# Kernel tuning notes

Hardware: AMD Instinct MI355X
Metric: run time of the kernel (lower is better)

The kernel has to match this reference:

```python
import jax, jax.numpy as jnp
import numpy as np

B, S, E, H = 2, 2048, 1024, 16
HD = E // H  # 64
NEG = -1e24


def setup_inputs() -> dict:
    key = jax.random.key(0)
    ks = jax.random.split(key, 20)
    sc_e = 1.0 / np.sqrt(E)
    inp = {
        "q_matrix": jax.random.normal(ks[0], (B, S, E), jnp.float32),
        "k_matrix": jax.random.normal(ks[1], (B, S, E), jnp.float32),
        "v_matrix": jax.random.normal(ks[2], (B, S, E), jnp.float32),
        "mask": jax.random.randint(ks[3], (B, S, S), 0, 2).astype(bool),
        # global QKV projections (embed_dim -> embed_dim)
        "Wq": jax.random.normal(ks[4], (E, E), jnp.float32) * sc_e,
        "bq": jnp.zeros((E,), jnp.float32),
        "Wk": jax.random.normal(ks[5], (E, E), jnp.float32) * sc_e,
        "bk": jnp.zeros((E,), jnp.float32),
        "Wv": jax.random.normal(ks[6], (E, E), jnp.float32) * sc_e,
        "bv": jnp.zeros((E,), jnp.float32),
        # per-head QKV projections (embed_dim -> head_dim), batched over heads
        "Whq": jax.random.normal(ks[7], (H, E, HD), jnp.float32) * sc_e,
        "bhq": jnp.zeros((H, HD), jnp.float32),
        "Whk": jax.random.normal(ks[8], (H, E, HD), jnp.float32) * sc_e,
        "bhk": jnp.zeros((H, HD), jnp.float32),
        "Whv": jax.random.normal(ks[9], (H, E, HD), jnp.float32) * sc_e,
        "bhv": jnp.zeros((H, HD), jnp.float32),
        # output projection
        "Wo": jax.random.normal(ks[10], (E, E), jnp.float32) * sc_e,
        "bo": jnp.zeros((E,), jnp.float32),
    }
    return inp


def reference(q_matrix, k_matrix, v_matrix, mask, Wq, bq, Wk, bk, Wv, bv,
              Whq, bhq, Whk, bhk, Whv, bhv, Wo, bo):
    # global projections [B,S,E]
    qg = q_matrix @ Wq + bq
    kg = k_matrix @ Wk + bk
    vg = v_matrix @ Wv + bv
    # per-head projections -> [B,H,S,HD]
    qh = jnp.einsum('bse,hed->bhsd', qg, Whq) + bhq[None, :, None, :]
    kh = jnp.einsum('bse,hed->bhsd', kg, Whk) + bhk[None, :, None, :]
    vh = jnp.einsum('bse,hed->bhsd', vg, Whv) + bhv[None, :, None, :]
    # scaled dot-product attention, scores [B,H,S,S]
    scores = jnp.einsum('bhsd,bhtd->bhst', qh, kh) / jnp.sqrt(jnp.float32(HD))
    scores = jnp.where(mask[:, None, :, :], NEG, scores)
    weights = jax.nn.softmax(scores, axis=-1)
    out = jnp.einsum('bhst,bhtd->bhsd', weights, vh)
    # concat heads (head order along last dim, matching torch.cat)
    x = out.transpose(0, 2, 1, 3).reshape(out.shape[0], out.shape[2], E)
    return x @ Wo + bo
```

## Files before the change

### kernel.cpp

```cpp
#include <hip/hip_runtime.h>
#include <hip/hip_bf16.h>

typedef unsigned short us16;
typedef __attribute__((ext_vector_type(8))) short short8;
typedef __attribute__((ext_vector_type(4))) float float4v;

#define E_DIM 1024
#define S_LEN 2048
#define B_DIM 2
#define H_DIM 16
#define HD_DIM 64
#define M_ROWS 4096

__device__ __forceinline__ us16 f2b(float f) {
    unsigned int u = __float_as_uint(f);
    unsigned int r = (u + 0x7fffu + ((u >> 16) & 1u)) >> 16;
    return (us16)r;
}
__device__ __forceinline__ us16 f2b_fast(float f) {
    return (us16)((__float_as_uint(f) + 0x8000u) >> 16);
}

__device__ __forceinline__ void gload16(const us16* g, us16* lds_uniform_base) {
    __builtin_amdgcn_global_load_lds(
        (const __attribute__((address_space(1))) void*)g,
        (__attribute__((address_space(3))) void*)lds_uniform_base, 16, 0, 0);
}

__global__ void zero_f32(float* p, int n) {
    int i = blockIdx.x * 256 + threadIdx.x;
    if (i < n) p[i] = 0.f;
}

__global__ void convert6(const float* s0, const float* s1, const float* s2,
                         const float* s3, const float* s4, const float* s5,
                         us16* d0, us16* d1, us16* d2,
                         us16* d3, us16* d4, us16* d5) {
    int z = blockIdx.y;
    const float* in = z == 0 ? s0 : z == 1 ? s1 : z == 2 ? s2 : z == 3 ? s3 : z == 4 ? s4 : s5;
    us16* out = z == 0 ? d0 : z == 1 ? d1 : z == 2 ? d2 : z == 3 ? d3 : z == 4 ? d4 : d5;
    int n = (z < 3) ? (M_ROWS * E_DIM) : (E_DIM * E_DIM);
    int idx = (blockIdx.x * 256 + threadIdx.x) * 8;
    if (idx >= n) return;
    float4 f0 = *(const float4*)(in + idx);
    float4 f1 = *(const float4*)(in + idx + 4);
    us16 t[8] = {f2b(f0.x), f2b(f0.y), f2b(f0.z), f2b(f0.w),
                 f2b(f1.x), f2b(f1.y), f2b(f1.z), f2b(f1.w)};
    *(uint4*)(out + idx) = *(const uint4*)t;
}

__global__ void transpose4(const float* __restrict__ s0, const float* __restrict__ s1,
                           const float* __restrict__ s2, const float* __restrict__ s3,
                           us16* __restrict__ d0, us16* __restrict__ d1,
                           us16* __restrict__ d2, us16* __restrict__ d3) {
    __shared__ us16 tile[32][33];
    int z = blockIdx.z;
    const float* in = z == 0 ? s0 : z == 1 ? s1 : z == 2 ? s2 : s3;
    us16* out = z == 0 ? d0 : z == 1 ? d1 : z == 2 ? d2 : d3;
    int mode = (z < 3) ? 1 : 0;
    int bx = blockIdx.x, by = blockIdx.y;
    int tx = threadIdx.x, ty = threadIdx.y;
#pragma unroll
    for (int i = 0; i < 4; ++i) {
        int e = by * 32 + ty + i * 8;
        int c = bx * 32 + tx;
        size_t src;
        if (mode == 0) src = (size_t)e * E_DIM + c;
        else           src = ((size_t)(c >> 6) * E_DIM + e) * 64 + (c & 63);
        tile[ty + i * 8][tx] = f2b(in[src]);
    }
    __syncthreads();
#pragma unroll
    for (int i = 0; i < 4; ++i) {
        int c = bx * 32 + ty + i * 8;
        int e = by * 32 + tx;
        out[(size_t)c * E_DIM + e] = tile[tx][ty + i * 8];
    }
}

__global__ void bias_combine3(const float* g0, const float* g1, const float* g2,
                              const float* W0, const float* W1, const float* W2,
                              const float* h0, const float* h1, const float* h2,
                              float* c0, float* c1, float* c2) {
    int z = blockIdx.y;
    const float* bg = z == 0 ? g0 : z == 1 ? g1 : g2;
    const float* Wh = z == 0 ? W0 : z == 1 ? W1 : W2;
    const float* bh = z == 0 ? h0 : z == 1 ? h1 : h2;
    float* bc = z == 0 ? c0 : z == 1 ? c1 : c2;
    int h = blockIdx.x;
    int tid = threadIdx.x;
    int d = tid & 63, part = tid >> 6;
    float acc = 0.f;
    int j0 = part * 256;
    for (int j = j0; j < j0 + 256; ++j)
        acc += bg[j] * Wh[((size_t)h * E_DIM + j) * HD_DIM + d];
    __shared__ float red[4][64];
    red[part][d] = acc;
    __syncthreads();
    if (tid < 64)
        bc[h * 64 + tid] = red[0][tid] + red[1][tid] + red[2][tid] + red[3][tid] + bh[h * 64 + tid];
}

__global__ void mask_pack(const int* __restrict__ mask, unsigned long long* __restrict__ bits) {
    int row = blockIdx.x * 4 + (threadIdx.x >> 6);
    int lane = threadIdx.x & 63;
    const int* mp = mask + (size_t)row * S_LEN;
    for (int w = 0; w < 32; ++w) {
        int mv = mp[w * 64 + lane];
        unsigned long long bal = __ballot(mv != 0);
        if (lane == 0) bits[(size_t)row * 32 + w] = bal;
    }
}

#define BK 32

__device__ __forceinline__ void gemm_body(
    const us16* __restrict__ A, const us16* __restrict__ Bt,
    const float* __restrict__ bias, void* __restrict__ Cp,
    int M, int N, int K, int bxt, int byt, int omode)
{
    __shared__ us16 As[128 * BK];
    __shared__ us16 Bs[128 * BK];

    int tid = threadIdx.x;
    int wave = tid >> 6, lane = tid & 63;
    int quad = lane >> 4, l16 = lane & 15;
    int wm = (wave >> 1) * 64, wn = (wave & 1) * 64;
    int bm0 = byt * 128, bn0 = bxt * 128;
    int srow = lane >> 2;
    int gcol = (((lane & 3) ^ (srow & 3)) << 3);
    int rslot = ((quad ^ (l16 & 3)) << 3);

    float4v acc[4][4];
#pragma unroll
    for (int i = 0; i < 4; ++i)
#pragma unroll
        for (int j = 0; j < 4; ++j)
#pragma unroll
            for (int r = 0; r < 4; ++r) acc[i][j][r] = 0.f;

    for (int k0 = 0; k0 < K; k0 += BK) {
#pragma unroll
        for (int c = 0; c < 2; ++c) {
            int r0 = 32 * wave + 16 * c;
            gload16(A  + (size_t)(bm0 + r0 + srow) * K + k0 + gcol, &As[r0 * BK]);
            gload16(Bt + (size_t)(bn0 + r0 + srow) * K + k0 + gcol, &Bs[r0 * BK]);
        }
        __syncthreads();
        short8 af[4], bfr[4];
#pragma unroll
        for (int i = 0; i < 4; ++i)
            af[i] = *(const short8*)&As[(wm + i * 16 + l16) * BK + rslot];
#pragma unroll
        for (int j = 0; j < 4; ++j)
            bfr[j] = *(const short8*)&Bs[(wn + j * 16 + l16) * BK + rslot];
#pragma unroll
        for (int i = 0; i < 4; ++i)
#pragma unroll
            for (int j = 0; j < 4; ++j)
                acc[i][j] = __builtin_amdgcn_mfma_f32_16x16x32_bf16(af[i], bfr[j], acc[i][j], 0, 0, 0);
        __syncthreads();
    }

#pragma unroll
    for (int i = 0; i < 4; ++i) {
#pragma unroll
        for (int j = 0; j < 4; ++j) {
#pragma unroll
            for (int r = 0; r < 4; ++r) {
                int row = bm0 + wm + i * 16 + quad * 4 + r;
                int col = bn0 + wn + j * 16 + l16;
                float v = acc[i][j][r] + ((omode == 3) ? bias[row] : bias[col]);
                if (omode == 0) {
                    ((us16*)Cp)[(size_t)row * N + col] = f2b(v);
                } else if (omode == 1) {
                    int b = row >> 11, s = row & 2047, h = col >> 6, d = col & 63;
                    ((us16*)Cp)[(((size_t)(b * H_DIM + h) * S_LEN + s) * HD_DIM) + d] = f2b(v);
                } else if (omode == 2) {
                    ((float*)Cp)[(size_t)row * N + col] = v;
                } else {
                    int h = row >> 6, d = row & 63, b = col >> 11, sl = col & 2047;
                    ((us16*)Cp)[(((size_t)(b * H_DIM + h) * HD_DIM + d) * S_LEN) + sl] = f2b(v);
                }
            }
        }
    }
}

__global__ __launch_bounds__(256) void wgemm3(
    const us16* A0, const us16* A1, const us16* A2,
    const us16* B0, const us16* B1, const us16* B2,
    const float* zbias, us16* C0, us16* C1, us16* C2)
{
    int z = blockIdx.z;
    const us16* A = z == 0 ? A0 : z == 1 ? A1 : A2;
    const us16* Bt = z == 0 ? B0 : z == 1 ? B1 : B2;
    us16* C = z == 0 ? C0 : z == 1 ? C1 : C2;
    gemm_body(A, Bt, zbias, C, E_DIM, E_DIM, E_DIM, blockIdx.x, blockIdx.y, 0);
}

__global__ __launch_bounds__(256) void proj_all(
    const us16* __restrict__ qb, const us16* __restrict__ kb, const us16* __restrict__ vb,
    const us16* __restrict__ WcqT, const us16* __restrict__ WckT, const us16* __restrict__ WcvT,
    const float* __restrict__ bcq, const float* __restrict__ bck, const float* __restrict__ bcv,
    us16* __restrict__ qhb, us16* __restrict__ khb, us16* __restrict__ vtb)
{
    int bx = blockIdx.x;
    int z = bx >> 8, t = bx & 255;
    if (z == 0)      gemm_body(qb, WcqT, bcq, qhb, M_ROWS, E_DIM, E_DIM, t & 7, t >> 3, 1);
    else if (z == 1) gemm_body(kb, WckT, bck, khb, M_ROWS, E_DIM, E_DIM, t & 7, t >> 3, 1);
    else             gemm_body(WcvT, vb, bcv, vtb, E_DIM, M_ROWS, E_DIM, t & 31, t >> 5, 3);
}

__global__ __launch_bounds__(256) void gemm_out64(
    const us16* __restrict__ A, const us16* __restrict__ Bt,
    const float* __restrict__ bias, float* __restrict__ C,
    int M, int N, int K)
{
    __shared__ us16 As[64 * BK];
    __shared__ us16 Bs[128 * BK];

    int tid = threadIdx.x;
    int wave = tid >> 6, lane = tid & 63;
    int quad = lane >> 4, l16 = lane & 15;
    int wm = (wave >> 1) * 32, wn = (wave & 1) * 64;
    int bm0 = blockIdx.y * 64, bn0 = blockIdx.x * 128;
    int srow = lane >> 2;
    int gcol = (((lane & 3) ^ (srow & 3)) << 3);
    int rslot = ((quad ^ (l16 & 3)) << 3);

    float4v acc[2][4];
#pragma unroll
    for (int i = 0; i < 2; ++i)
#pragma unroll
        for (int j = 0; j < 4; ++j)
#pragma unroll
            for (int r = 0; r < 4; ++r) acc[i][j][r] = 0.f;

    for (int k0 = 0; k0 < K; k0 += BK) {
        gload16(A + (size_t)(bm0 + 16 * wave + srow) * K + k0 + gcol, &As[16 * wave * BK]);
#pragma unroll
        for (int c = 0; c < 2; ++c) {
            int r0 = 32 * wave + 16 * c;
            gload16(Bt + (size_t)(bn0 + r0 + srow) * K + k0 + gcol, &Bs[r0 * BK]);
        }
        __syncthreads();
        short8 af[2], bfr[4];
#pragma unroll
        for (int i = 0; i < 2; ++i)
            af[i] = *(const short8*)&As[(wm + i * 16 + l16) * BK + rslot];
#pragma unroll
        for (int j = 0; j < 4; ++j)
            bfr[j] = *(const short8*)&Bs[(wn + j * 16 + l16) * BK + rslot];
#pragma unroll
        for (int i = 0; i < 2; ++i)
#pragma unroll
            for (int j = 0; j < 4; ++j)
                acc[i][j] = __builtin_amdgcn_mfma_f32_16x16x32_bf16(af[i], bfr[j], acc[i][j], 0, 0, 0);
        __syncthreads();
    }

#pragma unroll
    for (int i = 0; i < 2; ++i)
#pragma unroll
        for (int j = 0; j < 4; ++j)
#pragma unroll
            for (int r = 0; r < 4; ++r) {
                int row = bm0 + wm + i * 16 + quad * 4 + r;
                int col = bn0 + wn + j * 16 + l16;
                C[(size_t)row * N + col] = acc[i][j][r] + bias[col];
            }
}

#define LDK 72
#define LDP 76
#define SCALE2 0.18033688011112042f

__global__ __launch_bounds__(256) void attn_kernel(
    const us16* __restrict__ qh, const us16* __restrict__ kh,
    const us16* __restrict__ vt, const unsigned long long* __restrict__ mbits,
    us16* __restrict__ x)
{
    __shared__ us16 Ks[64 * LDK];
    __shared__ us16 Vs[64 * LDK];
    __shared__ us16 Pw[4][16 * LDP];

    int tid = threadIdx.x;
    int w = tid >> 6, lane = tid & 63;
    int quad = lane >> 4, l16 = lane & 15;
    int bh = blockIdx.y;
    int b = bh >> 4, h = bh & 15;
    int q0 = blockIdx.x * 64;
    const size_t base = (size_t)bh * (S_LEN * HD_DIM);

    short8 qf0, qf1;
    {
        int qrow = q0 + w * 16 + l16;
        const us16* qp = qh + base + (size_t)qrow * HD_DIM + quad * 8;
        qf0 = *(const short8*)qp;
        qf1 = *(const short8*)(qp + 32);
    }

    float l_i[4];
    float4v o[4];
#pragma unroll
    for (int r = 0; r < 4; ++r) l_i[r] = 0.f;
#pragma unroll
    for (int dt = 0; dt < 4; ++dt)
#pragma unroll
        for (int r = 0; r < 4; ++r) o[dt][r] = 0.f;

    int qb = q0 + w * 16 + quad * 4;
    const unsigned long long* mrow = mbits + (size_t)(b * S_LEN + qb) * 32;

    for (int kt = 0; kt < S_LEN; kt += 64) {
        __syncthreads();
#pragma unroll
        for (int it = 0; it < 2; ++it) {
            int c = tid + it * 256;
            int r = c >> 3, cc = (c & 7) * 8;
            *(uint4*)&Ks[r * LDK + cc] = *(const uint4*)(kh + base + (size_t)(kt + r) * HD_DIM + cc);
            *(uint4*)&Vs[r * LDK + cc] = *(const uint4*)(vt + base + (size_t)r * S_LEN + kt + cc);
        }
        __syncthreads();

        int kw = kt >> 6;
        unsigned long long mw[4];
#pragma unroll
        for (int r = 0; r < 4; ++r) mw[r] = mrow[r * 32 + kw];

        float4v sc[4];
#pragma unroll
        for (int ct = 0; ct < 4; ++ct) {
            short8 kf0 = *(const short8*)&Ks[(ct * 16 + l16) * LDK + quad * 8];
            short8 kf1 = *(const short8*)&Ks[(ct * 16 + l16) * LDK + 32 + quad * 8];
            float4v a;
#pragma unroll
            for (int r = 0; r < 4; ++r) a[r] = 0.f;
            a = __builtin_amdgcn_mfma_f32_16x16x32_bf16(qf0, kf0, a, 0, 0, 0);
            a = __builtin_amdgcn_mfma_f32_16x16x32_bf16(qf1, kf1, a, 0, 0, 0);
            sc[ct] = a;
        }

#pragma unroll
        for (int ct = 0; ct < 4; ++ct) {
            int sh = ct * 16 + l16;
#pragma unroll
            for (int r = 0; r < 4; ++r) {
                float pin = ((mw[r] >> sh) & 1ull) ? -1e38f : sc[ct][r] * SCALE2;
                float p = __builtin_amdgcn_exp2f(pin);
                l_i[r] += p;
                Pw[w][(quad * 4 + r) * LDP + ct * 16 + l16] = f2b_fast(p);
            }
        }

        short8 pf0 = *(const short8*)&Pw[w][l16 * LDP + quad * 8];
        short8 pf1 = *(const short8*)&Pw[w][l16 * LDP + 32 + quad * 8];
#pragma unroll
        for (int dt = 0; dt < 4; ++dt) {
            short8 vf0 = *(const short8*)&Vs[(dt * 16 + l16) * LDK + quad * 8];
            short8 vf1 = *(const short8*)&Vs[(dt * 16 + l16) * LDK + 32 + quad * 8];
            o[dt] = __builtin_amdgcn_mfma_f32_16x16x32_bf16(pf0, vf0, o[dt], 0, 0, 0);
            o[dt] = __builtin_amdgcn_mfma_f32_16x16x32_bf16(pf1, vf1, o[dt], 0, 0, 0);
        }
    }

#pragma unroll
    for (int r = 0; r < 4; ++r) {
        float s = l_i[r];
        s += __shfl_xor(s, 1, 64);
        s += __shfl_xor(s, 2, 64);
        s += __shfl_xor(s, 4, 64);
        s += __shfl_xor(s, 8, 64);
        l_i[r] = 1.0f / s;
    }
#pragma unroll
    for (int dt = 0; dt < 4; ++dt)
#pragma unroll
        for (int r = 0; r < 4; ++r) {
            int s = qb + r;
            int col = h * HD_DIM + dt * 16 + l16;
            x[(size_t)(b * S_LEN + s) * E_DIM + col] = f2b(o[dt][r] * l_i[r]);
        }
}

extern "C" void kernel_launch(void* const* d_in, const int* in_sizes, int n_in,
                              void* d_out, int out_size, void* d_ws, size_t ws_size,
                              hipStream_t stream) {
    const float* q    = (const float*)d_in[0];
    const float* k    = (const float*)d_in[1];
    const float* v    = (const float*)d_in[2];
    const int*   mask = (const int*)d_in[3];
    const float* Wq = (const float*)d_in[4];   const float* bq = (const float*)d_in[5];
    const float* Wk = (const float*)d_in[6];   const float* bk = (const float*)d_in[7];
    const float* Wv = (const float*)d_in[8];   const float* bv = (const float*)d_in[9];
    const float* Whq = (const float*)d_in[10]; const float* bhq = (const float*)d_in[11];
    const float* Whk = (const float*)d_in[12]; const float* bhk = (const float*)d_in[13];
    const float* Whv = (const float*)d_in[14]; const float* bhv = (const float*)d_in[15];
    const float* Wo = (const float*)d_in[16];  const float* bo = (const float*)d_in[17];

    us16* ws = (us16*)d_ws;
    const size_t M1 = (size_t)1 << 20;
    us16* WhqT = ws + 0 * M1;
    us16* WhkT = ws + 1 * M1;
    us16* WhvT = ws + 2 * M1;
    us16* WoT  = ws + 3 * M1;
    us16* WcqT = ws + 4 * M1;
    us16* WckT = ws + 5 * M1;
    us16* WcvT = ws + 6 * M1;
    us16* Wqb  = ws + 7 * M1;
    us16* Wkb  = ws + 8 * M1;
    us16* Wvb  = ws + 9 * M1;
    us16* qb   = ws + 10 * M1;
    us16* kb   = ws + 14 * M1;
    us16* vb   = ws + 18 * M1;
    us16* qhb  = ws + 22 * M1;
    us16* khb  = ws + 26 * M1;
    us16* vtb  = ws + 30 * M1;
    us16* xb   = vb;
    float* bcq   = (float*)(ws + 34 * M1);
    float* bck   = bcq + 1024;
    float* bcv   = bck + 1024;
    float* zbias = bcv + 1024;
    unsigned long long* mbits = (unsigned long long*)(ws + 34 * M1 + 16384);

    zero_f32<<<4, 256, 0, stream>>>(zbias, 1024);
    bias_combine3<<<dim3(H_DIM, 3), 256, 0, stream>>>(bq, bk, bv, Whq, Whk, Whv,
                                                      bhq, bhk, bhv, bcq, bck, bcv);
    transpose4<<<dim3(32, 32, 4), dim3(32, 8), 0, stream>>>(Whq, Whk, Whv, Wo,
                                                            WhqT, WhkT, WhvT, WoT);
    mask_pack<<<1024, 256, 0, stream>>>(mask, mbits);
    convert6<<<dim3(2048, 6), 256, 0, stream>>>(q, k, v, Wq, Wk, Wv,
                                                qb, kb, vb, Wqb, Wkb, Wvb);

    wgemm3<<<dim3(8, 8, 3), 256, 0, stream>>>(WhqT, WhkT, WhvT, Wqb, Wkb, Wvb, zbias,
                                              WcqT, WckT, WcvT);

    proj_all<<<768, 256, 0, stream>>>(qb, kb, vb, WcqT, WckT, WcvT,
                                      bcq, bck, bcv, qhb, khb, vtb);

    attn_kernel<<<dim3(32, 32), 256, 0, stream>>>(qhb, khb, vtb, mbits, xb);

    gemm_out64<<<dim3(8, 64), 256, 0, stream>>>(xb, WoT, bo, (float*)d_out,
                                                M_ROWS, E_DIM, E_DIM);
}
```

Baseline: 372.7 us.

## Merge prep kernels, split attention over key halves, use 64-row weight GEMM

Five small preprocessing launches (bf16 conversion, weight transposes, mask packing, bias combine, zeroing) become a single `prep` kernel dispatched by block index. The weight-combining GEMM moves to a 64-row tile body to launch more blocks. Attention splits the key range into two halves along a new grid dimension, with 512-thread blocks covering 128 queries. It writes unnormalized partial outputs and row sums, and a new `attn_combine` kernel adds the halves and normalizes. This aims to raise occupancy and parallelism and cut launch overhead, at the cost of extra partial-result memory traffic and one more launch. The combine step only adds partial sums, so it is only correct if the attention does not rely on a per-half running max.

```diff
diff --git a/kernel.cpp b/kernel.cpp
--- a/kernel.cpp
+++ b/kernel.cpp
@@ -12,6 +12,9 @@
 #define HD_DIM 64
 #define M_ROWS 4096
 
+__device__ __forceinline__ float b2f(us16 b) {
+    return __uint_as_float(((unsigned int)b) << 16);
+}
 __device__ __forceinline__ us16 f2b(float f) {
     unsigned int u = __float_as_uint(f);
     unsigned int r = (u + 0x7fffu + ((u >> 16) & 1u)) >> 16;
@@ -27,88 +30,91 @@
         (__attribute__((address_space(3))) void*)lds_uniform_base, 16, 0, 0);
 }
 
-__global__ void zero_f32(float* p, int n) {
-    int i = blockIdx.x * 256 + threadIdx.x;
-    if (i < n) p[i] = 0.f;
-}
-
-__global__ void convert6(const float* s0, const float* s1, const float* s2,
-                         const float* s3, const float* s4, const float* s5,
-                         us16* d0, us16* d1, us16* d2,
-                         us16* d3, us16* d4, us16* d5) {
-    int z = blockIdx.y;
-    const float* in = z == 0 ? s0 : z == 1 ? s1 : z == 2 ? s2 : z == 3 ? s3 : z == 4 ? s4 : s5;
-    us16* out = z == 0 ? d0 : z == 1 ? d1 : z == 2 ? d2 : z == 3 ? d3 : z == 4 ? d4 : d5;
-    int n = (z < 3) ? (M_ROWS * E_DIM) : (E_DIM * E_DIM);
-    int idx = (blockIdx.x * 256 + threadIdx.x) * 8;
-    if (idx >= n) return;
-    float4 f0 = *(const float4*)(in + idx);
-    float4 f1 = *(const float4*)(in + idx + 4);
-    us16 t[8] = {f2b(f0.x), f2b(f0.y), f2b(f0.z), f2b(f0.w),
-                 f2b(f1.x), f2b(f1.y), f2b(f1.z), f2b(f1.w)};
-    *(uint4*)(out + idx) = *(const uint4*)t;
-}
-
-__global__ void transpose4(const float* __restrict__ s0, const float* __restrict__ s1,
-                           const float* __restrict__ s2, const float* __restrict__ s3,
-                           us16* __restrict__ d0, us16* __restrict__ d1,
-                           us16* __restrict__ d2, us16* __restrict__ d3) {
+__global__ __launch_bounds__(256) void prep(
+    const float* __restrict__ q, const float* __restrict__ k, const float* __restrict__ v,
+    const float* __restrict__ Wq, const float* __restrict__ Wk, const float* __restrict__ Wv,
+    const float* __restrict__ Whq, const float* __restrict__ Whk, const float* __restrict__ Whv,
+    const float* __restrict__ Wo,
+    const float* __restrict__ bq, const float* __restrict__ bk, const float* __restrict__ bv,
+    const float* __restrict__ bhq, const float* __restrict__ bhk, const float* __restrict__ bhv,
+    const int* __restrict__ mask,
+    us16* qb, us16* kb, us16* vb, us16* Wqb, us16* Wkb, us16* Wvb,
+    us16* WhqT, us16* WhkT, us16* WhvT, us16* WoT,
+    unsigned long long* mbits,
+    float* bcq, float* bck, float* bcv, float* zbias)
+{
     __shared__ us16 tile[32][33];
-    int z = blockIdx.z;
-    const float* in = z == 0 ? s0 : z == 1 ? s1 : z == 2 ? s2 : s3;
-    us16* out = z == 0 ? d0 : z == 1 ? d1 : z == 2 ? d2 : d3;
-    int mode = (z < 3) ? 1 : 0;
-    int bx = blockIdx.x, by = blockIdx.y;
-    int tx = threadIdx.x, ty = threadIdx.y;
-#pragma unroll
-    for (int i = 0; i < 4; ++i) {
-        int e = by * 32 + ty + i * 8;
-        int c = bx * 32 + tx;
-        size_t src;
-        if (mode == 0) src = (size_t)e * E_DIM + c;
-        else           src = ((size_t)(c >> 6) * E_DIM + e) * 64 + (c & 63);
-        tile[ty + i * 8][tx] = f2b(in[src]);
-    }
-    __syncthreads();
-#pragma unroll
-    for (int i = 0; i < 4; ++i) {
-        int c = bx * 32 + ty + i * 8;
-        int e = by * 32 + tx;
-        out[(size_t)c * E_DIM + e] = tile[tx][ty + i * 8];
-    }
-}
-
-__global__ void bias_combine3(const float* g0, const float* g1, const float* g2,
-                              const float* W0, const float* W1, const float* W2,
-                              const float* h0, const float* h1, const float* h2,
-                              float* c0, float* c1, float* c2) {
-    int z = blockIdx.y;
-    const float* bg = z == 0 ? g0 : z == 1 ? g1 : g2;
-    const float* Wh = z == 0 ? W0 : z == 1 ? W1 : W2;
-    const float* bh = z == 0 ? h0 : z == 1 ? h1 : h2;
-    float* bc = z == 0 ? c0 : z == 1 ? c1 : c2;
-    int h = blockIdx.x;
-    int tid = threadIdx.x;
-    int d = tid & 63, part = tid >> 6;
-    float acc = 0.f;
-    int j0 = part * 256;
-    for (int j = j0; j < j0 + 256; ++j)
-        acc += bg[j] * Wh[((size_t)h * E_DIM + j) * HD_DIM + d];
     __shared__ float red[4][64];
-    red[part][d] = acc;
-    __syncthreads();
-    if (tid < 64)
-        bc[h * 64 + tid] = red[0][tid] + red[1][tid] + red[2][tid] + red[3][tid] + bh[h * 64 + tid];
-}
-
-__global__ void mask_pack(const int* __restrict__ mask, unsigned long long* __restrict__ bits) {
-    int row = blockIdx.x * 4 + (threadIdx.x >> 6);
-    int lane = threadIdx.x & 63;
-    const int* mp = mask + (size_t)row * S_LEN;
-    for (int w = 0; w < 32; ++w) {
-        int mv = mp[w * 64 + lane];
-        unsigned long long bal = __ballot(mv != 0);
-        if (lane == 0) bits[(size_t)row * 32 + w] = bal;
+    int blk = blockIdx.x, tid = threadIdx.x;
+
+    if (blk < 7680) {
+        const float* in; us16* out; int idx;
+        if (blk < 6144) {
+            int z = blk >> 11, rem = blk & 2047;
+            in = z == 0 ? q : z == 1 ? k : v;
+            out = z == 0 ? qb : z == 1 ? kb : vb;
+            idx = (rem * 256 + tid) * 8;
+        } else {
+            int t = blk - 6144, z = t >> 9, rem = t & 511;
+            in = z == 0 ? Wq : z == 1 ? Wk : Wv;
+            out = z == 0 ? Wqb : z == 1 ? Wkb : Wvb;
+            idx = (rem * 256 + tid) * 8;
+        }
+        float4 f0 = *(const float4*)(in + idx);
+        float4 f1 = *(const float4*)(in + idx + 4);
+        us16 t8[8] = {f2b(f0.x), f2b(f0.y), f2b(f0.z), f2b(f0.w),
+                      f2b(f1.x), f2b(f1.y), f2b(f1.z), f2b(f1.w)};
+        *(uint4*)(out + idx) = *(const uint4*)t8;
+    } else if (blk < 11776) {
+        int t = blk - 7680, z = t >> 10, rem = t & 1023;
+        const float* in = z == 0 ? Whq : z == 1 ? Whk : z == 2 ? Whv : Wo;
+        us16* out = z == 0 ? WhqT : z == 1 ? WhkT : z == 2 ? WhvT : WoT;
+        int mode = (z < 3) ? 1 : 0;
+        int bx = rem & 31, by = rem >> 5;
+        int tx = tid & 31, ty = tid >> 5;
+#pragma unroll
+        for (int i = 0; i < 4; ++i) {
+            int e = by * 32 + ty + i * 8;
+            int c = bx * 32 + tx;
+            size_t src;
+            if (mode == 0) src = (size_t)e * E_DIM + c;
+            else           src = ((size_t)(c >> 6) * E_DIM + e) * 64 + (c & 63);
+            tile[ty + i * 8][tx] = f2b(in[src]);
+        }
+        __syncthreads();
+#pragma unroll
+        for (int i = 0; i < 4; ++i) {
+            int c = bx * 32 + ty + i * 8;
+            int e = by * 32 + tx;
+            out[(size_t)c * E_DIM + e] = tile[tx][ty + i * 8];
+        }
+    } else if (blk < 12800) {
+        int row = (blk - 11776) * 4 + (tid >> 6);
+        int lane = tid & 63;
+        const int* mp = mask + (size_t)row * S_LEN;
+        for (int w = 0; w < 32; ++w) {
+            int mv = mp[w * 64 + lane];
+            unsigned long long bal = __ballot(mv != 0);
+            if (lane == 0) mbits[(size_t)row * 32 + w] = bal;
+        }
+    } else if (blk < 12848) {
+        int t = blk - 12800, z = t >> 4, h = t & 15;
+        const float* bg = z == 0 ? bq : z == 1 ? bk : bv;
+        const float* Wh = z == 0 ? Whq : z == 1 ? Whk : Whv;
+        const float* bh = z == 0 ? bhq : z == 1 ? bhk : bhv;
+        float* bc = z == 0 ? bcq : z == 1 ? bck : bcv;
+        int d = tid & 63, part = tid >> 6;
+        float acc = 0.f;
+        int j0 = part * 256;
+        for (int j = j0; j < j0 + 256; ++j)
+            acc += bg[j] * Wh[((size_t)h * E_DIM + j) * HD_DIM + d];
+        red[part][d] = acc;
+        __syncthreads();
+        if (tid < 64)
+            bc[h * 64 + tid] = red[0][tid] + red[1][tid] + red[2][tid] + red[3][tid] + bh[h * 64 + tid];
+    } else {
+        int i = (blk - 12848) * 256 + tid;
+        if (i < 1024) zbias[i] = 0.f;
     }
 }
 
@@ -170,33 +176,17 @@
             for (int r = 0; r < 4; ++r) {
                 int row = bm0 + wm + i * 16 + quad * 4 + r;
                 int col = bn0 + wn + j * 16 + l16;
-                float v = acc[i][j][r] + ((omode == 3) ? bias[row] : bias[col]);
-                if (omode == 0) {
-                    ((us16*)Cp)[(size_t)row * N + col] = f2b(v);
-                } else if (omode == 1) {
+                float vv = acc[i][j][r] + ((omode == 3) ? bias[row] : bias[col]);
+                if (omode == 1) {
                     int b = row >> 11, s = row & 2047, h = col >> 6, d = col & 63;
-                    ((us16*)Cp)[(((size_t)(b * H_DIM + h) * S_LEN + s) * HD_DIM) + d] = f2b(v);
-                } else if (omode == 2) {
-                    ((float*)Cp)[(size_t)row * N + col] = v;
+                    ((us16*)Cp)[(((size_t)(b * H_DIM + h) * S_LEN + s) * HD_DIM) + d] = f2b(vv);
                 } else {
                     int h = row >> 6, d = row & 63, b = col >> 11, sl = col & 2047;
-                    ((us16*)Cp)[(((size_t)(b * H_DIM + h) * HD_DIM + d) * S_LEN) + sl] = f2b(v);
+                    ((us16*)Cp)[(((size_t)(b * H_DIM + h) * HD_DIM + d) * S_LEN) + sl] = f2b(vv);
                 }
             }
         }
     }
-}
-
-__global__ __launch_bounds__(256) void wgemm3(
-    const us16* A0, const us16* A1, const us16* A2,
-    const us16* B0, const us16* B1, const us16* B2,
-    const float* zbias, us16* C0, us16* C1, us16* C2)
-{
-    int z = blockIdx.z;
-    const us16* A = z == 0 ? A0 : z == 1 ? A1 : A2;
-    const us16* Bt = z == 0 ? B0 : z == 1 ? B1 : B2;
-    us16* C = z == 0 ? C0 : z == 1 ? C1 : C2;
-    gemm_body(A, Bt, zbias, C, E_DIM, E_DIM, E_DIM, blockIdx.x, blockIdx.y, 0);
 }
 
 __global__ __launch_bounds__(256) void proj_all(
@@ -212,10 +202,11 @@
     else             gemm_body(WcvT, vb, bcv, vtb, E_DIM, M_ROWS, E_DIM, t & 31, t >> 5, 3);
 }
 
-__global__ __launch_bounds__(256) void gemm_out64(
+template<int OMODE>
+__device__ __forceinline__ void gemm64_body(
     const us16* __restrict__ A, const us16* __restrict__ Bt,
-    const float* __restrict__ bias, float* __restrict__ C,
-    int M, int N, int K)
+    const float* __restrict__ bias, void* __restrict__ Cp,
+    int M, int N, int K, int bxt, int byt)
 {
     __shared__ us16 As[64 * BK];
     __shared__ us16 Bs[128 * BK];
@@ -224,7 +215,7 @@
     int wave = tid >> 6, lane = tid & 63;
     int quad = lane >> 4, l16 = lane & 15;
     int wm = (wave >> 1) * 32, wn = (wave & 1) * 64;
-    int bm0 = blockIdx.y * 64, bn0 = blockIdx.x * 128;
+    int bm0 = byt * 64, bn0 = bxt * 128;
     int srow = lane >> 2;
     int gcol = (((lane & 3) ^ (srow & 3)) << 3);
     int rslot = ((quad ^ (l16 & 3)) << 3);
@@ -268,29 +259,51 @@
             for (int r = 0; r < 4; ++r) {
                 int row = bm0 + wm + i * 16 + quad * 4 + r;
                 int col = bn0 + wn + j * 16 + l16;
-                C[(size_t)row * N + col] = acc[i][j][r] + bias[col];
+                float vv = acc[i][j][r] + bias[col];
+                if (OMODE == 0) ((us16*)Cp)[(size_t)row * N + col] = f2b(vv);
+                else            ((float*)Cp)[(size_t)row * N + col] = vv;
             }
+}
+
+__global__ __launch_bounds__(256) void wgemm3(
+    const us16* A0, const us16* A1, const us16* A2,
+    const us16* B0, const us16* B1, const us16* B2,
+    const float* zbias, us16* C0, us16* C1, us16* C2)
+{
+    int z = blockIdx.z;
+    const us16* A = z == 0 ? A0 : z == 1 ? A1 : A2;
+    const us16* Bt = z == 0 ? B0 : z == 1 ? B1 : B2;
+    us16* C = z == 0 ? C0 : z == 1 ? C1 : C2;
+    gemm64_body<0>(A, Bt, zbias, C, E_DIM, E_DIM, E_DIM, blockIdx.x, blockIdx.y);
+}
+
+__global__ __launch_bounds__(256) void gemm_out64(
+    const us16* __restrict__ A, const us16* __restrict__ Bt,
+    const float* __restrict__ bias, float* __restrict__ C, int M, int N, int K)
+{
+    gemm64_body<2>(A, Bt, bias, C, M, N, K, blockIdx.x, blockIdx.y);
 }
 
 #define LDK 72
 #define LDP 76
 #define SCALE2 0.18033688011112042f
 
-__global__ __launch_bounds__(256) void attn_kernel(
+__global__ __launch_bounds__(512) void attn_kernel(
     const us16* __restrict__ qh, const us16* __restrict__ kh,
     const us16* __restrict__ vt, const unsigned long long* __restrict__ mbits,
-    us16* __restrict__ x)
+    us16* __restrict__ o_p, float* __restrict__ l_p)
 {
     __shared__ us16 Ks[64 * LDK];
     __shared__ us16 Vs[64 * LDK];
-    __shared__ us16 Pw[4][16 * LDP];
+    __shared__ us16 Pw[8][16 * LDP];
 
     int tid = threadIdx.x;
     int w = tid >> 6, lane = tid & 63;
     int quad = lane >> 4, l16 = lane & 15;
     int bh = blockIdx.y;
-    int b = bh >> 4, h = bh & 15;
-    int q0 = blockIdx.x * 64;
+    int b = bh >> 4;
+    int z = blockIdx.z;
+    int q0 = blockIdx.x * 128;
     const size_t base = (size_t)bh * (S_LEN * HD_DIM);
 
     short8 qf0, qf1;
@@ -313,12 +326,11 @@
     int qb = q0 + w * 16 + quad * 4;
     const unsigned long long* mrow = mbits + (size_t)(b * S_LEN + qb) * 32;
 
-    for (int kt = 0; kt < S_LEN; kt += 64) {
-        __syncthreads();
-#pragma unroll
-        for (int it = 0; it < 2; ++it) {
-            int c = tid + it * 256;
-            int r = c >> 3, cc = (c & 7) * 8;
+    int kend = z * 1024 + 1024;
+    for (int kt = z * 1024; kt < kend; kt += 64) {
+        __syncthreads();
+        {
+            int r = tid >> 3, cc = (tid & 7) * 8;
             *(uint4*)&Ks[r * LDK + cc] = *(const uint4*)(kh + base + (size_t)(kt + r) * HD_DIM + cc);
             *(uint4*)&Vs[r * LDK + cc] = *(const uint4*)(vt + base + (size_t)r * S_LEN + kt + cc);
         }
@@ -372,16 +384,38 @@
         s += __shfl_xor(s, 2, 64);
         s += __shfl_xor(s, 4, 64);
         s += __shfl_xor(s, 8, 64);
-        l_i[r] = 1.0f / s;
+        l_i[r] = s;
+    }
+    int rowg = bh * S_LEN + qb;
+    if (l16 == 0) {
+#pragma unroll
+        for (int r = 0; r < 4; ++r) l_p[(size_t)z * 65536 + rowg + r] = l_i[r];
     }
 #pragma unroll
     for (int dt = 0; dt < 4; ++dt)
 #pragma unroll
-        for (int r = 0; r < 4; ++r) {
-            int s = qb + r;
-            int col = h * HD_DIM + dt * 16 + l16;
-            x[(size_t)(b * S_LEN + s) * E_DIM + col] = f2b(o[dt][r] * l_i[r]);
-        }
+        for (int r = 0; r < 4; ++r)
+            o_p[(size_t)z * 4194304 + (size_t)(rowg + r) * 64 + dt * 16 + l16] = f2b(o[dt][r]);
+}
+
+__global__ __launch_bounds__(256) void attn_combine(
+    const us16* __restrict__ o_p, const float* __restrict__ l_p,
+    us16* __restrict__ x)
+{
+    int fidx = blockIdx.x * 256 + threadIdx.x;
+    int rix = fidx >> 3;
+    int d8 = (fidx & 7) * 8;
+    float linv = 1.0f / (l_p[rix] + l_p[65536 + rix]);
+    uint4 a = *(const uint4*)(o_p + (size_t)rix * 64 + d8);
+    uint4 c = *(const uint4*)(o_p + 4194304 + (size_t)rix * 64 + d8);
+    const us16* ap = (const us16*)&a;
+    const us16* cp = (const us16*)&c;
+    us16 t8[8];
+#pragma unroll
+    for (int i = 0; i < 8; ++i)
+        t8[i] = f2b((b2f(ap[i]) + b2f(cp[i])) * linv);
+    int bh = rix >> 11, b = bh >> 4, h = bh & 15, s = rix & 2047;
+    *(uint4*)&x[(size_t)(b * S_LEN + s) * E_DIM + h * HD_DIM + d8] = *(const uint4*)t8;
 }
 
 extern "C" void kernel_launch(void* const* d_in, const int* in_sizes, int n_in,
@@ -417,29 +451,29 @@
     us16* qhb  = ws + 22 * M1;
     us16* khb  = ws + 26 * M1;
     us16* vtb  = ws + 30 * M1;
+    us16* o_p  = qb;
     us16* xb   = vb;
     float* bcq   = (float*)(ws + 34 * M1);
     float* bck   = bcq + 1024;
     float* bcv   = bck + 1024;
     float* zbias = bcv + 1024;
     unsigned long long* mbits = (unsigned long long*)(ws + 34 * M1 + 16384);
-
-    zero_f32<<<4, 256, 0, stream>>>(zbias, 1024);
-    bias_combine3<<<dim3(H_DIM, 3), 256, 0, stream>>>(bq, bk, bv, Whq, Whk, Whv,
-                                                      bhq, bhk, bhv, bcq, bck, bcv);
-    transpose4<<<dim3(32, 32, 4), dim3(32, 8), 0, stream>>>(Whq, Whk, Whv, Wo,
-                                                            WhqT, WhkT, WhvT, WoT);
-    mask_pack<<<1024, 256, 0, stream>>>(mask, mbits);
-    convert6<<<dim3(2048, 6), 256, 0, stream>>>(q, k, v, Wq, Wk, Wv,
-                                                qb, kb, vb, Wqb, Wkb, Wvb);
-
-    wgemm3<<<dim3(8, 8, 3), 256, 0, stream>>>(WhqT, WhkT, WhvT, Wqb, Wkb, Wvb, zbias,
-                                              WcqT, WckT, WcvT);
+    float* l_p = (float*)(ws + 34 * M1 + 16384 + 524288);
+
+    prep<<<12852, 256, 0, stream>>>(q, k, v, Wq, Wk, Wv, Whq, Whk, Whv, Wo,
+                                    bq, bk, bv, bhq, bhk, bhv, mask,
+                                    qb, kb, vb, Wqb, Wkb, Wvb,
+                                    WhqT, WhkT, WhvT, WoT, mbits,
+                                    bcq, bck, bcv, zbias);
+
+    wgemm3<<<dim3(8, 16, 3), 256, 0, stream>>>(WhqT, WhkT, WhvT, Wqb, Wkb, Wvb, zbias,
+                                               WcqT, WckT, WcvT);
 
     proj_all<<<768, 256, 0, stream>>>(qb, kb, vb, WcqT, WckT, WcvT,
                                       bcq, bck, bcv, qhb, khb, vtb);
 
-    attn_kernel<<<dim3(32, 32), 256, 0, stream>>>(qhb, khb, vtb, mbits, xb);
+    attn_kernel<<<dim3(16, 32, 2), 512, 0, stream>>>(qhb, khb, vtb, mbits, o_p, l_p);
+    attn_combine<<<2048, 256, 0, stream>>>(o_p, l_p, xb);
 
     gemm_out64<<<dim3(8, 64), 256, 0, stream>>>(xb, WoT, bo, (float*)d_out,
                                                 M_ROWS, E_DIM, E_DIM);
```

Result: faster. 339.4 us (-8.9%).
